# Optimization experiments

Measured on AMD Instinct MI355X. Metric: run time of the kernel, lower is better.

## Reference

```python
import jax, jax.numpy as jnp
import numpy as np

EMBED_DIM = 2048
NUM_Q_HEADS = 16
HEAD_DIM = EMBED_DIM // NUM_Q_HEADS  # 128
SCALE = 1.0 / np.sqrt(EMBED_DIM)     # note: module uses 1/sqrt(embed_dim)
B, S = 4, 2048


def setup_inputs() -> dict:
    key = jax.random.key(0)
    ks = jax.random.split(key, 9)
    sd = 0.02
    return {
        "x": jax.random.normal(ks[0], (B, S, EMBED_DIM), dtype=jnp.float32),
        "Wq": jax.random.normal(ks[1], (EMBED_DIM, EMBED_DIM), dtype=jnp.float32) * sd,
        "bq": jnp.zeros((EMBED_DIM,), dtype=jnp.float32),
        "Wk": jax.random.normal(ks[2], (HEAD_DIM, EMBED_DIM), dtype=jnp.float32) * sd,
        "bk": jnp.zeros((HEAD_DIM,), dtype=jnp.float32),
        "Wv": jax.random.normal(ks[3], (HEAD_DIM, EMBED_DIM), dtype=jnp.float32) * sd,
        "bv": jnp.zeros((HEAD_DIM,), dtype=jnp.float32),
        "Wo": jax.random.normal(ks[4], (EMBED_DIM, EMBED_DIM), dtype=jnp.float32) * sd,
        "bo": jnp.zeros((EMBED_DIM,), dtype=jnp.float32),
    }


def reference(x, Wq, bq, Wk, bk, Wv, bv, Wo, bo):
    b, s, _ = x.shape
    # projections (nn.Linear: y = x @ W.T + b)
    q = (x @ Wq.T + bq).reshape(b, s, NUM_Q_HEADS, HEAD_DIM)  # [b,s,h,d]
    k = x @ Wk.T + bk   # [b,t,d] single KV head (MQA)
    v = x @ Wv.T + bv   # [b,t,d]
    # SDPA with single K/V head broadcast across all query heads
    scores = jnp.einsum("bshd,btd->bhst", q, k) * SCALE  # [b,h,s,t]
    attn = jax.nn.softmax(scores, axis=-1)
    out = jnp.einsum("bhst,btd->bshd", attn, v).reshape(b, s, EMBED_DIM)
    return out @ Wo.T + bo
```

## Files before the change

kernel.cpp:

```cpp
#include <hip/hip_runtime.h>
#include <stdint.h>
#include <cmath>

#define B_ 4
#define S_ 2048
#define E_ 2048
#define H_ 16
#define D_ 128
#define M_ (B_*S_)

typedef unsigned short u16;
typedef __attribute__((ext_vector_type(8))) short short8;
typedef __attribute__((ext_vector_type(4))) float f32x4;

__device__ __forceinline__ u16 f2bf(float f) {
  union { float f; uint32_t u; } v; v.f = f;
  uint32_t r = v.u + 0x7fffu + ((v.u >> 16) & 1u);
  return (u16)(r >> 16);
}

__device__ __forceinline__ float exp2_fast(float x) {
  float r; asm("v_exp_f32 %0, %1" : "=v"(r) : "v"(x)); return r;
}

__device__ __forceinline__ uint32_t cvtpk_bf16(float lo, float hi) {
  uint32_t r; asm("v_cvt_pk_bf16_f32 %0, %1, %2" : "=v"(r) : "v"(lo), "v"(hi));
  return r;
}

__device__ __forceinline__ void async16(const void* g, void* s) {
  __builtin_amdgcn_global_load_lds(
      (const __attribute__((address_space(1))) uint32_t*)g,
      (__attribute__((address_space(3))) uint32_t*)s, 16, 0, 0);
}

#define XSEG   4194304L
#define WQSEG  1048576L
#define WKSEG    65536L
__global__ __launch_bounds__(256) void cvt_all(
    const float4* __restrict__ x,  const float4* __restrict__ wq,
    const float4* __restrict__ wk, const float4* __restrict__ wv,
    const float4* __restrict__ wo,
    ushort4* __restrict__ xb,  ushort4* __restrict__ wqb,
    ushort4* __restrict__ wkb, ushort4* __restrict__ wvb,
    ushort4* __restrict__ wob) {
  long i = (long)blockIdx.x * 256 + threadIdx.x;
  const float4* src; ushort4* dst; long off;
  if (i < XSEG)                            { src = x;  dst = xb;  off = 0; }
  else if (i < XSEG + WQSEG)               { src = wq; dst = wqb; off = XSEG; }
  else if (i < XSEG + WQSEG + WKSEG)       { src = wk; dst = wkb; off = XSEG + WQSEG; }
  else if (i < XSEG + WQSEG + 2*WKSEG)     { src = wv; dst = wvb; off = XSEG + WQSEG + WKSEG; }
  else                                     { src = wo; dst = wob; off = XSEG + WQSEG + 2*WKSEG; }
  long j = i - off;
  float4 v = src[j];
  ushort4 o;
  o.x = f2bf(v.x); o.y = f2bf(v.y); o.z = f2bf(v.z); o.w = f2bf(v.w);
  dst[j] = o;
}

template<int OUT>
__global__ __launch_bounds__(512, 2) void gemm256(
    const u16* __restrict__ A, const u16* __restrict__ Bm,
    const float* __restrict__ bias, void* __restrict__ Cout,
    int Ndim, int K, float oscale) {
  __shared__ u16 lA[2][2][128*64];
  __shared__ u16 lB[2][2][128*64];
  const int tid = threadIdx.x;
  const int l = tid & 63, w = tid >> 6;
  const int lr = l & 15, lg = l >> 4;
  const int wm = w >> 2, wn = w & 3;

  const int bid = blockIdx.y * 8 + blockIdx.x;
  const int xcd = bid & 7, ii = bid >> 3;
  const int brow = (xcd >> 1) * 8 + (ii >> 2);
  const int bcol = (xcd & 1) * 4 + (ii & 3);
  const int row0A = brow * 256;
  const int row0B = bcol * 256;

  f32x4 acc[8][4] = {};
  const int nk = K >> 6;

  auto STG = [&](u16* dst, const u16* src, int k0) {
    #pragma unroll
    for (int c = 0; c < 2; ++c) {
      int idx = c*512 + tid;
      int r = idx >> 3, ch = idx & 7;
      async16(src + (size_t)r*K + k0 + (ch ^ (r & 7))*8,
              dst + (size_t)(c*512 + w*64)*8);
    }
  };
  auto SLOT = [&](int t, int s) {
    if (t >= nk) return;
    int d = t & 1;
    if (s < 2) STG(&lA[d][s][0],   A  + (size_t)(row0A + s*128)*K,     t*64);
    else       STG(&lB[d][s-2][0], Bm + (size_t)(row0B + (s-2)*128)*K, t*64);
  };
  auto rdA = [&](int d, int i, int ks) -> short8 {
    int ra = i*16 + lr;
    return *(const short8*)((const char*)&lA[d][wm][0] +
           ((ra*128 + ks*64 + lg*16) ^ ((ra & 7) << 4)));
  };
  auto rdB = [&](int d, int j, int ks) -> short8 {
    int rb = (wn & 1)*64 + j*16 + lr;
    return *(const short8*)((const char*)&lB[d][wn >> 1][0] +
           ((rb*128 + ks*64 + lg*16) ^ ((rb & 7) << 4)));
  };
  auto BAR = [] { __builtin_amdgcn_s_barrier(); asm volatile("" ::: "memory"); };

  short8 afr[4][2], bfr[4][2];

  SLOT(0, 0); SLOT(0, 1); SLOT(0, 2); SLOT(0, 3);
  SLOT(1, 0);
  asm volatile("s_waitcnt vmcnt(2)" ::: "memory");
  BAR();

  const int niter = nk >> 1;
  for (int n = 0; n < niter; ++n) {
    const bool lastit = (n == niter - 1);
    const int t1 = 2*n + 1;

    #pragma unroll
    for (int i2 = 0; i2 < 4; ++i2)
      #pragma unroll
      for (int ks = 0; ks < 2; ++ks) afr[i2][ks] = rdA(0, i2, ks);
    #pragma unroll
    for (int j = 0; j < 2; ++j)
      #pragma unroll
      for (int ks = 0; ks < 2; ++ks) bfr[j][ks] = rdB(0, j, ks);
    SLOT(t1, 1);
    BAR();
    __builtin_amdgcn_s_setprio(1);
    #pragma unroll
    for (int i2 = 0; i2 < 4; ++i2)
      #pragma unroll
      for (int j = 0; j < 2; ++j)
        #pragma unroll
        for (int ks = 0; ks < 2; ++ks)
          acc[i2][j] = __builtin_amdgcn_mfma_f32_16x16x32_bf16(
                         afr[i2][ks], bfr[j][ks], acc[i2][j], 0, 0, 0);
    __builtin_amdgcn_s_setprio(0);
    BAR();

    #pragma unroll
    for (int j = 2; j < 4; ++j)
      #pragma unroll
      for (int ks = 0; ks < 2; ++ks) bfr[j][ks] = rdB(0, j, ks);
    SLOT(t1, 2);
    BAR();
    __builtin_amdgcn_s_setprio(1);
    #pragma unroll
    for (int i2 = 0; i2 < 4; ++i2)
      #pragma unroll
      for (int j = 2; j < 4; ++j)
        #pragma unroll
        for (int ks = 0; ks < 2; ++ks)
          acc[i2][j] = __builtin_amdgcn_mfma_f32_16x16x32_bf16(
                         afr[i2][ks], bfr[j][ks], acc[i2][j], 0, 0, 0);
    __builtin_amdgcn_s_setprio(0);
    BAR();

    #pragma unroll
    for (int i2 = 0; i2 < 4; ++i2)
      #pragma unroll
      for (int ks = 0; ks < 2; ++ks) afr[i2][ks] = rdA(0, 4 + i2, ks);
    SLOT(t1, 3);
    BAR();
    __builtin_amdgcn_s_setprio(1);
    #pragma unroll
    for (int i2 = 0; i2 < 4; ++i2)
      #pragma unroll
      for (int j = 0; j < 2; ++j)
        #pragma unroll
        for (int ks = 0; ks < 2; ++ks)
          acc[4 + i2][j] = __builtin_amdgcn_mfma_f32_16x16x32_bf16(
                             afr[i2][ks], bfr[j][ks], acc[4 + i2][j], 0, 0, 0);
    __builtin_amdgcn_s_setprio(0);
    BAR();

    SLOT(2*n + 2, 0);
    BAR();
    __builtin_amdgcn_s_setprio(1);
    #pragma unroll
    for (int i2 = 0; i2 < 4; ++i2)
      #pragma unroll
      for (int j = 2; j < 4; ++j)
        #pragma unroll
        for (int ks = 0; ks < 2; ++ks)
          acc[4 + i2][j] = __builtin_amdgcn_mfma_f32_16x16x32_bf16(
                             afr[i2][ks], bfr[j][ks], acc[4 + i2][j], 0, 0, 0);
    __builtin_amdgcn_s_setprio(0);
    if (lastit) asm volatile("s_waitcnt vmcnt(0)" ::: "memory");
    else        asm volatile("s_waitcnt vmcnt(2)" ::: "memory");
    BAR();

    #pragma unroll
    for (int i2 = 0; i2 < 4; ++i2)
      #pragma unroll
      for (int ks = 0; ks < 2; ++ks) afr[i2][ks] = rdA(1, i2, ks);
    #pragma unroll
    for (int j = 0; j < 2; ++j)
      #pragma unroll
      for (int ks = 0; ks < 2; ++ks) bfr[j][ks] = rdB(1, j, ks);
    SLOT(2*n + 2, 1);
    BAR();
    __builtin_amdgcn_s_setprio(1);
    #pragma unroll
    for (int i2 = 0; i2 < 4; ++i2)
      #pragma unroll
      for (int j = 0; j < 2; ++j)
        #pragma unroll
        for (int ks = 0; ks < 2; ++ks)
          acc[i2][j] = __builtin_amdgcn_mfma_f32_16x16x32_bf16(
                         afr[i2][ks], bfr[j][ks], acc[i2][j], 0, 0, 0);
    __builtin_amdgcn_s_setprio(0);
    BAR();

    #pragma unroll
    for (int j = 2; j < 4; ++j)
      #pragma unroll
      for (int ks = 0; ks < 2; ++ks) bfr[j][ks] = rdB(1, j, ks);
    SLOT(2*n + 2, 2);
    BAR();
    __builtin_amdgcn_s_setprio(1);
    #pragma unroll
    for (int i2 = 0; i2 < 4; ++i2)
      #pragma unroll
      for (int j = 2; j < 4; ++j)
        #pragma unroll
        for (int ks = 0; ks < 2; ++ks)
          acc[i2][j] = __builtin_amdgcn_mfma_f32_16x16x32_bf16(
                         afr[i2][ks], bfr[j][ks], acc[i2][j], 0, 0, 0);
    __builtin_amdgcn_s_setprio(0);
    BAR();

    #pragma unroll
    for (int i2 = 0; i2 < 4; ++i2)
      #pragma unroll
      for (int ks = 0; ks < 2; ++ks) afr[i2][ks] = rdA(1, 4 + i2, ks);
    SLOT(2*n + 2, 3);
    BAR();
    __builtin_amdgcn_s_setprio(1);
    #pragma unroll
    for (int i2 = 0; i2 < 4; ++i2)
      #pragma unroll
      for (int j = 0; j < 2; ++j)
        #pragma unroll
        for (int ks = 0; ks < 2; ++ks)
          acc[4 + i2][j] = __builtin_amdgcn_mfma_f32_16x16x32_bf16(
                             afr[i2][ks], bfr[j][ks], acc[4 + i2][j], 0, 0, 0);
    __builtin_amdgcn_s_setprio(0);
    BAR();

    SLOT(2*n + 3, 0);
    BAR();
    __builtin_amdgcn_s_setprio(1);
    #pragma unroll
    for (int i2 = 0; i2 < 4; ++i2)
      #pragma unroll
      for (int j = 2; j < 4; ++j)
        #pragma unroll
        for (int ks = 0; ks < 2; ++ks)
          acc[4 + i2][j] = __builtin_amdgcn_mfma_f32_16x16x32_bf16(
                             afr[i2][ks], bfr[j][ks], acc[4 + i2][j], 0, 0, 0);
    __builtin_amdgcn_s_setprio(0);
    if (lastit) asm volatile("s_waitcnt vmcnt(0)" ::: "memory");
    else        asm volatile("s_waitcnt vmcnt(2)" ::: "memory");
    BAR();
  }

  const int crow0 = row0A + wm*128;
  const int ccol0 = row0B + wn*64;
  #pragma unroll
  for (int j = 0; j < 4; ++j) {
    int col = ccol0 + j*16 + lr;
    float bv = bias[col];
    #pragma unroll
    for (int i = 0; i < 8; ++i) {
      #pragma unroll
      for (int r = 0; r < 4; ++r) {
        int row = crow0 + i*16 + lg*4 + r;
        float vo = (acc[i][j][r] + bv) * oscale;
        if (OUT == 0) ((float*)Cout)[(size_t)row*Ndim + col] = vo;
        else          ((u16*)Cout)[(size_t)row*Ndim + col] = f2bf(vo);
      }
    }
  }
}

__global__ __launch_bounds__(256) void gemm_kv(
    const u16* __restrict__ A, const u16* __restrict__ Wkb, const u16* __restrict__ Wvb,
    const float* __restrict__ bkp, const float* __restrict__ bvp,
    u16* __restrict__ kout, u16* __restrict__ vTout) {
  __shared__ u16 lA[128*64];
  __shared__ u16 lB[128*64];
  const int tid = threadIdx.x;
  const int l = tid & 63, w = tid >> 6;
  const int lr = l & 15, lg = l >> 4;
  const int wr = w >> 1, wc = w & 1;
  const int row0A = blockIdx.y * 128;
  const bool isV = (blockIdx.x != 0);
  const u16* Bm = isV ? Wvb : Wkb;
  const float* bias = isV ? bvp : bkp;

  f32x4 acc[4][4] = {};

  for (int k0 = 0; k0 < E_; k0 += 64) {
    __syncthreads();
    #pragma unroll
    for (int c = 0; c < 4; ++c) {
      int idx = c*256 + tid;
      int r = idx >> 3, ch = idx & 7;
      async16(A + (size_t)(row0A + r)*E_ + k0 + (ch ^ (r & 7))*8,
              lA + (size_t)(c*256 + w*64)*8);
    }
    #pragma unroll
    for (int c = 0; c < 4; ++c) {
      int idx = c*256 + tid;
      int r = idx >> 3, ch = idx & 7;
      async16(Bm + (size_t)r*E_ + k0 + (ch ^ (r & 7))*8,
              lB + (size_t)(c*256 + w*64)*8);
    }
    __syncthreads();
    #pragma unroll
    for (int ks = 0; ks < 2; ++ks) {
      short8 af[4], bfr[4];
      #pragma unroll
      for (int i = 0; i < 4; ++i) {
        int ra = wr*64 + i*16 + lr;
        af[i] = *(const short8*)((const char*)lA +
                 ((ra*128 + ks*64 + lg*16) ^ ((ra & 7) << 4)));
        int rb = wc*64 + i*16 + lr;
        bfr[i] = *(const short8*)((const char*)lB +
                 ((rb*128 + ks*64 + lg*16) ^ ((rb & 7) << 4)));
      }
      #pragma unroll
      for (int i = 0; i < 4; ++i)
        #pragma unroll
        for (int j = 0; j < 4; ++j)
          acc[i][j] = __builtin_amdgcn_mfma_f32_16x16x32_bf16(
                        af[i], bfr[j], acc[i][j], 0, 0, 0);
    }
  }

  const int crow0 = row0A + wr*64;
  #pragma unroll
  for (int j = 0; j < 4; ++j) {
    int col = wc*64 + j*16 + lr;
    float bvv = bias[col];
    #pragma unroll
    for (int i = 0; i < 4; ++i) {
      #pragma unroll
      for (int r = 0; r < 4; ++r) {
        int row = crow0 + i*16 + lg*4 + r;
        float vo = acc[i][j][r] + bvv;
        if (isV) vTout[(size_t)col*M_ + row] = f2bf(vo);
        else     kout[(size_t)row*D_ + col] = f2bf(vo);
      }
    }
  }
}

__global__ __launch_bounds__(512) void mqa_flash(
    const u16* __restrict__ q, const u16* __restrict__ k,
    const u16* __restrict__ vT, u16* __restrict__ o) {
  __shared__ u16 lKbuf[2][64*128];
  __shared__ u16 lVbuf[2][128*64];

  const int tid = threadIdx.x;
  const int l = tid & 63, w = tid >> 6;
  const int lr = l & 15, lg = l >> 4;
  const int qt = blockIdx.x, b = blockIdx.z;
  const int h = blockIdx.y*2 + (w >> 2);
  const int qrow0 = b*S_ + qt*128 + (w & 3)*32;

  short8 qf[2][4];
  #pragma unroll
  for (int st = 0; st < 2; ++st) {
    const u16* qp = q + (size_t)(qrow0 + st*16 + lr)*E_ + h*D_;
    #pragma unroll
    for (int ks = 0; ks < 4; ++ks)
      qf[st][ks] = *(const short8*)(qp + ks*32 + lg*8);
  }

  short8 ones;
  #pragma unroll
  for (int j = 0; j < 8; ++j) ones[j] = (short)0x3F80;

  f32x4 oa[2][8];
  f32x4 la[2] = {f32x4{0.f,0.f,0.f,0.f}, f32x4{0.f,0.f,0.f,0.f}};
  #pragma unroll
  for (int st = 0; st < 2; ++st)
    #pragma unroll
    for (int dn = 0; dn < 8; ++dn) oa[st][dn] = f32x4{0.f,0.f,0.f,0.f};

  const u16* kbase = k + (size_t)b*S_*D_;
  const u16* vbase = vT + (size_t)b*S_;
  char* lK0 = (char*)&lKbuf[0][0];
  char* lV0 = (char*)&lVbuf[0][0];

  auto STAGE = [&](int off, int tt) {
    #pragma unroll
    for (int c = 0; c < 2; ++c) {
      int idx = c*512 + tid;
      int s = idx >> 4, ch = idx & 15;
      int pr = (s & 32) | ((s & 12) << 1) | ((s & 16) >> 2) | (s & 3);
      async16(kbase + (size_t)(tt + pr)*D_ + (ch ^ (s & 7))*8,
              lK0 + off + (size_t)(c*512 + w*64)*16);
    }
    #pragma unroll
    for (int c = 0; c < 2; ++c) {
      int idx = c*512 + tid;
      int r = idx >> 3, ch = idx & 7;
      async16(vbase + (size_t)r*M_ + tt + (ch ^ (r & 7))*8,
              lV0 + off + (size_t)(c*512 + w*64)*16);
    }
  };

  STAGE(0, 0);
  __syncthreads();
  int roff = 0;

  for (int t0 = 0; t0 < S_; t0 += 64) {
    const int woff = roff ^ 16384;
    if (t0 + 64 < S_) STAGE(woff, t0 + 64);

    const char* lKc = lK0 + roff;
    const char* lVc = lV0 + roff;

    f32x4 sa[2][4];
    #pragma unroll
    for (int st = 0; st < 2; ++st)
      #pragma unroll
      for (int n = 0; n < 4; ++n) sa[st][n] = f32x4{0.f,0.f,0.f,0.f};
    __builtin_amdgcn_s_setprio(1);
    #pragma unroll
    for (int n = 0; n < 4; ++n)
      #pragma unroll
      for (int ks = 0; ks < 4; ++ks) {
        short8 kf = *(const short8*)(lKc +
                    (((n*16 + lr)*256 + ks*64 + lg*16) ^ ((lr & 7) << 4)));
        sa[0][n] = __builtin_amdgcn_mfma_f32_16x16x32_bf16(kf, qf[0][ks], sa[0][n], 0, 0, 0);
        sa[1][n] = __builtin_amdgcn_mfma_f32_16x16x32_bf16(kf, qf[1][ks], sa[1][n], 0, 0, 0);
      }
    __builtin_amdgcn_s_setprio(0);

    short8 pa[2][2];
    #pragma unroll
    for (int st = 0; st < 2; ++st) {
      #pragma unroll
      for (int n = 0; n < 4; ++n)
        #pragma unroll
        for (int r = 0; r < 4; ++r)
          sa[st][n][r] = exp2_fast(sa[st][n][r]);
      #pragma unroll
      for (int ks = 0; ks < 2; ++ks) {
        union { short8 s8; uint32_t u[4]; } pu;
        pu.u[0] = cvtpk_bf16(sa[st][2*ks  ][0], sa[st][2*ks  ][1]);
        pu.u[1] = cvtpk_bf16(sa[st][2*ks  ][2], sa[st][2*ks  ][3]);
        pu.u[2] = cvtpk_bf16(sa[st][2*ks+1][0], sa[st][2*ks+1][1]);
        pu.u[3] = cvtpk_bf16(sa[st][2*ks+1][2], sa[st][2*ks+1][3]);
        pa[st][ks] = pu.s8;
      }
    }

    __builtin_amdgcn_s_setprio(1);
    la[0] = __builtin_amdgcn_mfma_f32_16x16x32_bf16(pa[0][0], ones, la[0], 0, 0, 0);
    la[0] = __builtin_amdgcn_mfma_f32_16x16x32_bf16(pa[0][1], ones, la[0], 0, 0, 0);
    la[1] = __builtin_amdgcn_mfma_f32_16x16x32_bf16(pa[1][0], ones, la[1], 0, 0, 0);
    la[1] = __builtin_amdgcn_mfma_f32_16x16x32_bf16(pa[1][1], ones, la[1], 0, 0, 0);

    #pragma unroll
    for (int dn = 0; dn < 8; ++dn)
      #pragma unroll
      for (int ks = 0; ks < 2; ++ks) {
        short8 vf = *(const short8*)(lVc +
                    (((dn*16 + lr)*128 + ks*64 + lg*16) ^ ((lr & 7) << 4)));
        oa[0][dn] = __builtin_amdgcn_mfma_f32_16x16x32_bf16(pa[0][ks], vf, oa[0][dn], 0, 0, 0);
        oa[1][dn] = __builtin_amdgcn_mfma_f32_16x16x32_bf16(pa[1][ks], vf, oa[1][dn], 0, 0, 0);
      }
    __builtin_amdgcn_s_setprio(0);

    __syncthreads();
    roff = woff;
  }

  #pragma unroll
  for (int st = 0; st < 2; ++st) {
    #pragma unroll
    for (int r = 0; r < 4; ++r) {
      float inv = 1.0f / la[st][r];
      u16* orow = o + (size_t)(qrow0 + st*16 + lg*4 + r)*E_ + h*D_ + lr;
      #pragma unroll
      for (int dn = 0; dn < 8; ++dn)
        orow[dn*16] = f2bf(oa[st][dn][r] * inv);
    }
  }
}

extern "C" void kernel_launch(void* const* d_in, const int* in_sizes, int n_in,
                              void* d_out, int out_size, void* d_ws, size_t ws_size,
                              hipStream_t stream) {
  (void)in_sizes; (void)n_in; (void)out_size; (void)ws_size;
  const float* x  = (const float*)d_in[0];
  const float* Wq = (const float*)d_in[1];
  const float* bq = (const float*)d_in[2];
  const float* Wk = (const float*)d_in[3];
  const float* bk = (const float*)d_in[4];
  const float* Wv = (const float*)d_in[5];
  const float* bv = (const float*)d_in[6];
  const float* Wo = (const float*)d_in[7];
  const float* bo = (const float*)d_in[8];
  float* out = (float*)d_out;

  char* ws = (char*)d_ws;
  u16* xb  = (u16*)(ws + 0);
  u16* qb  = (u16*)(ws + 33554432);
  u16* kb  = (u16*)(ws + 67108864);
  u16* vbT = (u16*)(ws + 69206016);
  u16* Wqb = (u16*)(ws + 71303168);
  u16* Wkb = (u16*)(ws + 79691776);
  u16* Wvb = (u16*)(ws + 80216064);
  u16* Wob = (u16*)(ws + 80740352);
  u16* ob  = xb;

  cvt_all<<<25088, 256, 0, stream>>>(
      (const float4*)x, (const float4*)Wq, (const float4*)Wk,
      (const float4*)Wv, (const float4*)Wo,
      (ushort4*)xb, (ushort4*)Wqb, (ushort4*)Wkb, (ushort4*)Wvb, (ushort4*)Wob);

  gemm_kv<<<dim3(2, M_/128), 256, 0, stream>>>(xb, Wkb, Wvb, bk, bv, kb, vbT);

  float qsc = 1.44269504088896f / sqrtf((float)E_);
  gemm256<1><<<dim3(E_/256, M_/256), 512, 0, stream>>>(xb, Wqb, bq, qb, E_, E_, qsc);

  mqa_flash<<<dim3(S_/128, H_/2, B_), 512, 0, stream>>>(qb, kb, vbT, ob);

  gemm256<0><<<dim3(E_/256, M_/256), 512, 0, stream>>>(ob, Wob, bo, out, E_, E_, 1.0f);
}
```

Measured before the change: 341.8 us.

## Give each flash-attention wave 64 query rows of one head to reuse K/V fragments

Each attention block now covers 512 query rows of a single head, and each wave holds 64 rows (four 16-row strips) instead of 32. Each K and V fragment read from LDS therefore feeds four MFMAs instead of two, halving LDS read traffic per FLOP. The key tile is processed in two 32-column phases to bound register pressure for the scores. Launch bounds now request two blocks per CU. The larger accumulators (4x8 output tiles) raise VGPR use and may cap occupancy, and the grid shrinks to 256 blocks.

```diff
diff --git a/kernel.cpp b/kernel.cpp
--- a/kernel.cpp
+++ b/kernel.cpp
@@ -360,7 +360,7 @@
   }
 }
 
-__global__ __launch_bounds__(512) void mqa_flash(
+__global__ __launch_bounds__(512, 2) void mqa_flash(
     const u16* __restrict__ q, const u16* __restrict__ k,
     const u16* __restrict__ vT, u16* __restrict__ o) {
   __shared__ u16 lKbuf[2][64*128];
@@ -369,13 +369,12 @@
   const int tid = threadIdx.x;
   const int l = tid & 63, w = tid >> 6;
   const int lr = l & 15, lg = l >> 4;
-  const int qt = blockIdx.x, b = blockIdx.z;
-  const int h = blockIdx.y*2 + (w >> 2);
-  const int qrow0 = b*S_ + qt*128 + (w & 3)*32;
-
-  short8 qf[2][4];
+  const int qt = blockIdx.x, h = blockIdx.y, b = blockIdx.z;
+  const int qrow0 = b*S_ + qt*512 + w*64;
+
+  short8 qf[4][4];
   #pragma unroll
-  for (int st = 0; st < 2; ++st) {
+  for (int st = 0; st < 4; ++st) {
     const u16* qp = q + (size_t)(qrow0 + st*16 + lr)*E_ + h*D_;
     #pragma unroll
     for (int ks = 0; ks < 4; ++ks)
@@ -386,10 +385,11 @@
   #pragma unroll
   for (int j = 0; j < 8; ++j) ones[j] = (short)0x3F80;
 
-  f32x4 oa[2][8];
-  f32x4 la[2] = {f32x4{0.f,0.f,0.f,0.f}, f32x4{0.f,0.f,0.f,0.f}};
+  f32x4 oa[4][8];
+  f32x4 la[4] = {f32x4{0.f,0.f,0.f,0.f}, f32x4{0.f,0.f,0.f,0.f},
+                 f32x4{0.f,0.f,0.f,0.f}, f32x4{0.f,0.f,0.f,0.f}};
   #pragma unroll
-  for (int st = 0; st < 2; ++st)
+  for (int st = 0; st < 4; ++st)
     #pragma unroll
     for (int dn = 0; dn < 8; ++dn) oa[st][dn] = f32x4{0.f,0.f,0.f,0.f};
 
@@ -427,65 +427,68 @@
     const char* lKc = lK0 + roff;
     const char* lVc = lV0 + roff;
 
-    f32x4 sa[2][4];
-    #pragma unroll
-    for (int st = 0; st < 2; ++st)
-      #pragma unroll
-      for (int n = 0; n < 4; ++n) sa[st][n] = f32x4{0.f,0.f,0.f,0.f};
-    __builtin_amdgcn_s_setprio(1);
-    #pragma unroll
-    for (int n = 0; n < 4; ++n)
+    #pragma unroll
+    for (int ph = 0; ph < 2; ++ph) {
+      f32x4 s0[4], s1[4];
+      #pragma unroll
+      for (int st = 0; st < 4; ++st) {
+        s0[st] = f32x4{0.f,0.f,0.f,0.f};
+        s1[st] = f32x4{0.f,0.f,0.f,0.f};
+      }
+      __builtin_amdgcn_s_setprio(1);
       #pragma unroll
       for (int ks = 0; ks < 4; ++ks) {
-        short8 kf = *(const short8*)(lKc +
-                    (((n*16 + lr)*256 + ks*64 + lg*16) ^ ((lr & 7) << 4)));
-        sa[0][n] = __builtin_amdgcn_mfma_f32_16x16x32_bf16(kf, qf[0][ks], sa[0][n], 0, 0, 0);
-        sa[1][n] = __builtin_amdgcn_mfma_f32_16x16x32_bf16(kf, qf[1][ks], sa[1][n], 0, 0, 0);
-      }
-    __builtin_amdgcn_s_setprio(0);
-
-    short8 pa[2][2];
-    #pragma unroll
-    for (int st = 0; st < 2; ++st) {
-      #pragma unroll
-      for (int n = 0; n < 4; ++n)
-        #pragma unroll
-        for (int r = 0; r < 4; ++r)
-          sa[st][n][r] = exp2_fast(sa[st][n][r]);
-      #pragma unroll
-      for (int ks = 0; ks < 2; ++ks) {
+        short8 kf0 = *(const short8*)(lKc +
+            ((((2*ph  )*16 + lr)*256 + ks*64 + lg*16) ^ ((lr & 7) << 4)));
+        short8 kf1 = *(const short8*)(lKc +
+            ((((2*ph+1)*16 + lr)*256 + ks*64 + lg*16) ^ ((lr & 7) << 4)));
+        #pragma unroll
+        for (int st = 0; st < 4; ++st)
+          s0[st] = __builtin_amdgcn_mfma_f32_16x16x32_bf16(kf0, qf[st][ks], s0[st], 0, 0, 0);
+        #pragma unroll
+        for (int st = 0; st < 4; ++st)
+          s1[st] = __builtin_amdgcn_mfma_f32_16x16x32_bf16(kf1, qf[st][ks], s1[st], 0, 0, 0);
+      }
+      __builtin_amdgcn_s_setprio(0);
+
+      short8 pa[4];
+      #pragma unroll
+      for (int st = 0; st < 4; ++st) {
+        #pragma unroll
+        for (int r = 0; r < 4; ++r) {
+          s0[st][r] = exp2_fast(s0[st][r]);
+          s1[st][r] = exp2_fast(s1[st][r]);
+        }
         union { short8 s8; uint32_t u[4]; } pu;
-        pu.u[0] = cvtpk_bf16(sa[st][2*ks  ][0], sa[st][2*ks  ][1]);
-        pu.u[1] = cvtpk_bf16(sa[st][2*ks  ][2], sa[st][2*ks  ][3]);
-        pu.u[2] = cvtpk_bf16(sa[st][2*ks+1][0], sa[st][2*ks+1][1]);
-        pu.u[3] = cvtpk_bf16(sa[st][2*ks+1][2], sa[st][2*ks+1][3]);
-        pa[st][ks] = pu.s8;
-      }
-    }
-
-    __builtin_amdgcn_s_setprio(1);
-    la[0] = __builtin_amdgcn_mfma_f32_16x16x32_bf16(pa[0][0], ones, la[0], 0, 0, 0);
-    la[0] = __builtin_amdgcn_mfma_f32_16x16x32_bf16(pa[0][1], ones, la[0], 0, 0, 0);
-    la[1] = __builtin_amdgcn_mfma_f32_16x16x32_bf16(pa[1][0], ones, la[1], 0, 0, 0);
-    la[1] = __builtin_amdgcn_mfma_f32_16x16x32_bf16(pa[1][1], ones, la[1], 0, 0, 0);
-
-    #pragma unroll
-    for (int dn = 0; dn < 8; ++dn)
-      #pragma unroll
-      for (int ks = 0; ks < 2; ++ks) {
+        pu.u[0] = cvtpk_bf16(s0[st][0], s0[st][1]);
+        pu.u[1] = cvtpk_bf16(s0[st][2], s0[st][3]);
+        pu.u[2] = cvtpk_bf16(s1[st][0], s1[st][1]);
+        pu.u[3] = cvtpk_bf16(s1[st][2], s1[st][3]);
+        pa[st] = pu.s8;
+      }
+
+      __builtin_amdgcn_s_setprio(1);
+      #pragma unroll
+      for (int st = 0; st < 4; ++st)
+        la[st] = __builtin_amdgcn_mfma_f32_16x16x32_bf16(pa[st], ones, la[st], 0, 0, 0);
+
+      #pragma unroll
+      for (int dn = 0; dn < 8; ++dn) {
         short8 vf = *(const short8*)(lVc +
-                    (((dn*16 + lr)*128 + ks*64 + lg*16) ^ ((lr & 7) << 4)));
-        oa[0][dn] = __builtin_amdgcn_mfma_f32_16x16x32_bf16(pa[0][ks], vf, oa[0][dn], 0, 0, 0);
-        oa[1][dn] = __builtin_amdgcn_mfma_f32_16x16x32_bf16(pa[1][ks], vf, oa[1][dn], 0, 0, 0);
-      }
-    __builtin_amdgcn_s_setprio(0);
+            (((dn*16 + lr)*128 + ph*64 + lg*16) ^ ((lr & 7) << 4)));
+        #pragma unroll
+        for (int st = 0; st < 4; ++st)
+          oa[st][dn] = __builtin_amdgcn_mfma_f32_16x16x32_bf16(pa[st], vf, oa[st][dn], 0, 0, 0);
+      }
+      __builtin_amdgcn_s_setprio(0);
+    }
 
     __syncthreads();
     roff = woff;
   }
 
   #pragma unroll
-  for (int st = 0; st < 2; ++st) {
+  for (int st = 0; st < 4; ++st) {
     #pragma unroll
     for (int r = 0; r < 4; ++r) {
       float inv = 1.0f / la[st][r];
@@ -533,7 +536,7 @@
   float qsc = 1.44269504088896f / sqrtf((float)E_);
   gemm256<1><<<dim3(E_/256, M_/256), 512, 0, stream>>>(xb, Wqb, bq, qb, E_, E_, qsc);
 
-  mqa_flash<<<dim3(S_/128, H_/2, B_), 512, 0, stream>>>(qb, kb, vbT, ob);
+  mqa_flash<<<dim3(S_/512, H_, B_), 512, 0, stream>>>(qb, kb, vbT, ob);
 
   gemm256<0><<<dim3(E_/256, M_/256), 512, 0, stream>>>(ob, Wob, bo, out, E_, E_, 1.0f);
 }
```

New measurement: 426.6 us. 1.25x slower.

## Fuse K/V projection into Q GEMM and read V fragments directly from global

Applied to the files above, without the earlier changes.

The separate K/V projection kernel is removed. Its work becomes a ninth column tile of the Q-projection GEMM, which relies on Wk and Wv being contiguous in the workspace, with the epilogue writing K row-major and V transposed. This saves a launch and a second full pass over x. In the attention kernel, V is no longer staged through LDS: each wave loads V fragments from global memory with one-step prefetching across the output column loop. That frees LDS and issue slots, but risks cache-dependent latency on strided vT loads that every wave repeats.

```diff
diff --git a/kernel.cpp b/kernel.cpp
--- a/kernel.cpp
+++ b/kernel.cpp
@@ -58,11 +58,14 @@
   dst[j] = o;
 }
 
-template<int OUT>
+template<int MODE>
 __global__ __launch_bounds__(512, 2) void gemm256(
-    const u16* __restrict__ A, const u16* __restrict__ Bm,
-    const float* __restrict__ bias, void* __restrict__ Cout,
-    int Ndim, int K, float oscale) {
+    const u16* __restrict__ A, const u16* __restrict__ Bq,
+    const u16* __restrict__ Bkv,
+    const float* __restrict__ bias0, const float* __restrict__ bkp,
+    const float* __restrict__ bvp,
+    void* __restrict__ C0, u16* __restrict__ kout, u16* __restrict__ vTout,
+    int K, float oscale) {
   __shared__ u16 lA[2][2][128*64];
   __shared__ u16 lB[2][2][128*64];
   const int tid = threadIdx.x;
@@ -70,12 +73,20 @@
   const int lr = l & 15, lg = l >> 4;
   const int wm = w >> 2, wn = w & 3;
 
-  const int bid = blockIdx.y * 8 + blockIdx.x;
-  const int xcd = bid & 7, ii = bid >> 3;
-  const int brow = (xcd >> 1) * 8 + (ii >> 2);
-  const int bcol = (xcd & 1) * 4 + (ii & 3);
+  const int bid = blockIdx.y * gridDim.x + blockIdx.x;
+  int brow, bcol;
+  if (MODE == 0) {
+    int xcd = bid & 7, ii = bid >> 3;
+    brow = (xcd >> 1) * 8 + (ii >> 2);
+    bcol = (xcd & 1) * 4 + (ii & 3);
+  } else {
+    int xcd = bid & 7, ii = bid >> 3;
+    brow = xcd * 4 + ii / 9;
+    bcol = ii % 9;
+  }
+  const bool iskv = (MODE == 1) && (bcol == 8);
+  const u16* Bsrc = iskv ? Bkv : (Bq + (size_t)bcol * 256 * K);
   const int row0A = brow * 256;
-  const int row0B = bcol * 256;
 
   f32x4 acc[8][4] = {};
   const int nk = K >> 6;
@@ -92,8 +103,8 @@
   auto SLOT = [&](int t, int s) {
     if (t >= nk) return;
     int d = t & 1;
-    if (s < 2) STG(&lA[d][s][0],   A  + (size_t)(row0A + s*128)*K,     t*64);
-    else       STG(&lB[d][s-2][0], Bm + (size_t)(row0B + (s-2)*128)*K, t*64);
+    if (s < 2) STG(&lA[d][s][0],   A    + (size_t)(row0A + s*128)*K, t*64);
+    else       STG(&lB[d][s-2][0], Bsrc + (size_t)((s-2)*128)*K,     t*64);
   };
   auto rdA = [&](int d, int i, int ks) -> short8 {
     int ra = i*16 + lr;
@@ -269,92 +280,25 @@
   }
 
   const int crow0 = row0A + wm*128;
-  const int ccol0 = row0B + wn*64;
   #pragma unroll
   for (int j = 0; j < 4; ++j) {
-    int col = ccol0 + j*16 + lr;
-    float bv = bias[col];
+    int lc = wn*64 + j*16 + lr;
     #pragma unroll
     for (int i = 0; i < 8; ++i) {
       #pragma unroll
       for (int r = 0; r < 4; ++r) {
         int row = crow0 + i*16 + lg*4 + r;
-        float vo = (acc[i][j][r] + bv) * oscale;
-        if (OUT == 0) ((float*)Cout)[(size_t)row*Ndim + col] = vo;
-        else          ((u16*)Cout)[(size_t)row*Ndim + col] = f2bf(vo);
-      }
-    }
-  }
-}
-
-__global__ __launch_bounds__(256) void gemm_kv(
-    const u16* __restrict__ A, const u16* __restrict__ Wkb, const u16* __restrict__ Wvb,
-    const float* __restrict__ bkp, const float* __restrict__ bvp,
-    u16* __restrict__ kout, u16* __restrict__ vTout) {
-  __shared__ u16 lA[128*64];
-  __shared__ u16 lB[128*64];
-  const int tid = threadIdx.x;
-  const int l = tid & 63, w = tid >> 6;
-  const int lr = l & 15, lg = l >> 4;
-  const int wr = w >> 1, wc = w & 1;
-  const int row0A = blockIdx.y * 128;
-  const bool isV = (blockIdx.x != 0);
-  const u16* Bm = isV ? Wvb : Wkb;
-  const float* bias = isV ? bvp : bkp;
-
-  f32x4 acc[4][4] = {};
-
-  for (int k0 = 0; k0 < E_; k0 += 64) {
-    __syncthreads();
-    #pragma unroll
-    for (int c = 0; c < 4; ++c) {
-      int idx = c*256 + tid;
-      int r = idx >> 3, ch = idx & 7;
-      async16(A + (size_t)(row0A + r)*E_ + k0 + (ch ^ (r & 7))*8,
-              lA + (size_t)(c*256 + w*64)*8);
-    }
-    #pragma unroll
-    for (int c = 0; c < 4; ++c) {
-      int idx = c*256 + tid;
-      int r = idx >> 3, ch = idx & 7;
-      async16(Bm + (size_t)r*E_ + k0 + (ch ^ (r & 7))*8,
-              lB + (size_t)(c*256 + w*64)*8);
-    }
-    __syncthreads();
-    #pragma unroll
-    for (int ks = 0; ks < 2; ++ks) {
-      short8 af[4], bfr[4];
-      #pragma unroll
-      for (int i = 0; i < 4; ++i) {
-        int ra = wr*64 + i*16 + lr;
-        af[i] = *(const short8*)((const char*)lA +
-                 ((ra*128 + ks*64 + lg*16) ^ ((ra & 7) << 4)));
-        int rb = wc*64 + i*16 + lr;
-        bfr[i] = *(const short8*)((const char*)lB +
-                 ((rb*128 + ks*64 + lg*16) ^ ((rb & 7) << 4)));
-      }
-      #pragma unroll
-      for (int i = 0; i < 4; ++i)
-        #pragma unroll
-        for (int j = 0; j < 4; ++j)
-          acc[i][j] = __builtin_amdgcn_mfma_f32_16x16x32_bf16(
-                        af[i], bfr[j], acc[i][j], 0, 0, 0);
-    }
-  }
-
-  const int crow0 = row0A + wr*64;
-  #pragma unroll
-  for (int j = 0; j < 4; ++j) {
-    int col = wc*64 + j*16 + lr;
-    float bvv = bias[col];
-    #pragma unroll
-    for (int i = 0; i < 4; ++i) {
-      #pragma unroll
-      for (int r = 0; r < 4; ++r) {
-        int row = crow0 + i*16 + lg*4 + r;
-        float vo = acc[i][j][r] + bvv;
-        if (isV) vTout[(size_t)col*M_ + row] = f2bf(vo);
-        else     kout[(size_t)row*D_ + col] = f2bf(vo);
+        float a = acc[i][j][r];
+        if (MODE == 0) {
+          ((float*)C0)[(size_t)row*E_ + bcol*256 + lc] = a + bias0[bcol*256 + lc];
+        } else if (!iskv) {
+          ((u16*)C0)[(size_t)row*E_ + bcol*256 + lc] =
+              f2bf((a + bias0[bcol*256 + lc]) * oscale);
+        } else if (lc < 128) {
+          kout[(size_t)row*D_ + lc] = f2bf(a + bkp[lc]);
+        } else {
+          vTout[(size_t)(lc - 128)*M_ + row] = f2bf(a + bvp[lc - 128]);
+        }
       }
     }
   }
@@ -364,7 +308,6 @@
     const u16* __restrict__ q, const u16* __restrict__ k,
     const u16* __restrict__ vT, u16* __restrict__ o) {
   __shared__ u16 lKbuf[2][64*128];
-  __shared__ u16 lVbuf[2][128*64];
 
   const int tid = threadIdx.x;
   const int l = tid & 63, w = tid >> 6;
@@ -396,7 +339,6 @@
   const u16* kbase = k + (size_t)b*S_*D_;
   const u16* vbase = vT + (size_t)b*S_;
   char* lK0 = (char*)&lKbuf[0][0];
-  char* lV0 = (char*)&lVbuf[0][0];
 
   auto STAGE = [&](int off, int tt) {
     #pragma unroll
@@ -407,13 +349,6 @@
       async16(kbase + (size_t)(tt + pr)*D_ + (ch ^ (s & 7))*8,
               lK0 + off + (size_t)(c*512 + w*64)*16);
     }
-    #pragma unroll
-    for (int c = 0; c < 2; ++c) {
-      int idx = c*512 + tid;
-      int r = idx >> 3, ch = idx & 7;
-      async16(vbase + (size_t)r*M_ + tt + (ch ^ (r & 7))*8,
-              lV0 + off + (size_t)(c*512 + w*64)*16);
-    }
   };
 
   STAGE(0, 0);
@@ -425,7 +360,6 @@
     if (t0 + 64 < S_) STAGE(woff, t0 + 64);
 
     const char* lKc = lK0 + roff;
-    const char* lVc = lV0 + roff;
 
     f32x4 sa[2][4];
     #pragma unroll
@@ -443,6 +377,10 @@
         sa[1][n] = __builtin_amdgcn_mfma_f32_16x16x32_bf16(kf, qf[1][ks], sa[1][n], 0, 0, 0);
       }
     __builtin_amdgcn_s_setprio(0);
+
+    const u16* vrow = vbase + t0;
+    short8 vfa = *(const short8*)(vrow + (size_t)lr*M_ + lg*8);
+    short8 vfb = *(const short8*)(vrow + (size_t)lr*M_ + 32 + lg*8);
 
     short8 pa[2][2];
     #pragma unroll
@@ -470,14 +408,18 @@
     la[1] = __builtin_amdgcn_mfma_f32_16x16x32_bf16(pa[1][1], ones, la[1], 0, 0, 0);
 
     #pragma unroll
-    for (int dn = 0; dn < 8; ++dn)
-      #pragma unroll
-      for (int ks = 0; ks < 2; ++ks) {
-        short8 vf = *(const short8*)(lVc +
-                    (((dn*16 + lr)*128 + ks*64 + lg*16) ^ ((lr & 7) << 4)));
-        oa[0][dn] = __builtin_amdgcn_mfma_f32_16x16x32_bf16(pa[0][ks], vf, oa[0][dn], 0, 0, 0);
-        oa[1][dn] = __builtin_amdgcn_mfma_f32_16x16x32_bf16(pa[1][ks], vf, oa[1][dn], 0, 0, 0);
+    for (int dn = 0; dn < 8; ++dn) {
+      short8 nfa = vfa, nfb = vfb;
+      if (dn < 7) {
+        nfa = *(const short8*)(vrow + (size_t)((dn+1)*16 + lr)*M_ + lg*8);
+        nfb = *(const short8*)(vrow + (size_t)((dn+1)*16 + lr)*M_ + 32 + lg*8);
       }
+      oa[0][dn] = __builtin_amdgcn_mfma_f32_16x16x32_bf16(pa[0][0], vfa, oa[0][dn], 0, 0, 0);
+      oa[1][dn] = __builtin_amdgcn_mfma_f32_16x16x32_bf16(pa[1][0], vfa, oa[1][dn], 0, 0, 0);
+      oa[0][dn] = __builtin_amdgcn_mfma_f32_16x16x32_bf16(pa[0][1], vfb, oa[0][dn], 0, 0, 0);
+      oa[1][dn] = __builtin_amdgcn_mfma_f32_16x16x32_bf16(pa[1][1], vfb, oa[1][dn], 0, 0, 0);
+      vfa = nfa; vfb = nfb;
+    }
     __builtin_amdgcn_s_setprio(0);
 
     __syncthreads();
@@ -528,12 +470,12 @@
       (const float4*)Wv, (const float4*)Wo,
       (ushort4*)xb, (ushort4*)Wqb, (ushort4*)Wkb, (ushort4*)Wvb, (ushort4*)Wob);
 
-  gemm_kv<<<dim3(2, M_/128), 256, 0, stream>>>(xb, Wkb, Wvb, bk, bv, kb, vbT);
-
   float qsc = 1.44269504088896f / sqrtf((float)E_);
-  gemm256<1><<<dim3(E_/256, M_/256), 512, 0, stream>>>(xb, Wqb, bq, qb, E_, E_, qsc);
+  gemm256<1><<<dim3(9, 32), 512, 0, stream>>>(
+      xb, Wqb, Wkb, bq, bk, bv, qb, kb, vbT, E_, qsc);
 
   mqa_flash<<<dim3(S_/128, H_/2, B_), 512, 0, stream>>>(qb, kb, vbT, ob);
 
-  gemm256<0><<<dim3(E_/256, M_/256), 512, 0, stream>>>(ob, Wob, bo, out, E_, E_, 1.0f);
-}
+  gemm256<0><<<dim3(8, 32), 512, 0, stream>>>(
+      ob, Wob, nullptr, bo, nullptr, nullptr, out, nullptr, nullptr, E_, 1.0f);
+}
```

Result: slower. 542.5 us (+58.7%).
